# Optimization experiments

Measured on AMD Instinct MI355X. Metric: run time of the kernel, lower is better.

## Reference

```python
import jax, jax.numpy as jnp
import numpy as np


def _segment_mean(msg, dst, num_nodes):
    # msg: [E, B, O, T] summed into [N, B, O, T], mean over incoming edges
    s = jax.ops.segment_sum(msg, dst, num_segments=num_nodes)
    cnt = jax.ops.segment_sum(jnp.ones((msg.shape[0],), msg.dtype), dst, num_segments=num_nodes)
    return s / jnp.clip(cnt, 1.0)[:, None, None, None]


def _gcn(x, edge_index, edge_attr, A, Wk, Wr, b):
    # Edge-conditioned (spline-style) graph conv.
    # x: [B, N, Cin, T]; edge_attr: [E, 3]; Wk: [K, Cin, Cout]
    N = x.shape[1]
    src, dst = edge_index[0], edge_index[1]
    Bw = jax.nn.softmax(edge_attr @ A, axis=-1)          # [E, K] basis weights
    We = jnp.einsum('ek,kio->eio', Bw, Wk)                # [E, Cin, Cout]
    msg = jnp.einsum('beit,eio->ebot', x[:, src], We)     # [E, B, Cout, T]
    agg = _segment_mean(msg, dst, N).transpose(1, 0, 2, 3)  # [B, N, Cout, T]
    out = agg + jnp.einsum('bnit,io->bnot', x, Wr) + b[None, None, :, None]
    return jax.nn.elu(out)


def _pool(x, P, C, T):
    # x: [B, N_l, C, T] -> flatten, sparse-pool with P [N_{l+1}, N_l], unflatten
    B, N = x.shape[0], x.shape[1]
    xf = x.reshape(B, N, C * T)
    xf = jnp.einsum('mn,bnf->bmf', P, xf)
    return xf.reshape(B, P.shape[0], C, T)


def setup_inputs() -> dict:
    key = jax.random.key(0)
    ks = jax.random.split(key, 24)
    B, T = 2, 200
    N = [2048, 512, 128, 64]
    E = [16384, 8192, 2048]
    nf = [1, 8, 16, 32, 64, 128, 128]
    ld = 64

    def rn(k, shape, scale=1.0):
        return jax.random.normal(k, shape, dtype=jnp.float32) * scale

    inp = {}
    inp['x'] = rn(ks[0], (B, N[0], nf[0], T))
    inp['ei0'] = jax.random.randint(ks[1], (2, E[0]), 0, N[0])
    inp['ea0'] = jax.random.uniform(ks[2], (E[0], 3), dtype=jnp.float32)
    inp['ei1'] = jax.random.randint(ks[3], (2, E[1]), 0, N[1])
    inp['ea1'] = jax.random.uniform(ks[4], (E[1], 3), dtype=jnp.float32)
    inp['ei2'] = jax.random.randint(ks[5], (2, E[2]), 0, N[2])
    inp['ea2'] = jax.random.uniform(ks[6], (E[2], 3), dtype=jnp.float32)
    # gcn params: (A basis map, K=3 kernel weights, root weight, bias)
    inp['A1'] = rn(ks[7], (3, 3))
    inp['Wk1'] = rn(ks[8], (3, nf[0], nf[2]), 1.0 / np.sqrt(nf[0]))
    inp['Wr1'] = rn(ks[9], (nf[0], nf[2]), 1.0 / np.sqrt(nf[0]))
    inp['b1'] = jnp.zeros((nf[2],), jnp.float32)
    inp['A2'] = rn(ks[10], (3, 3))
    inp['Wk2'] = rn(ks[11], (3, nf[2], nf[3]), 1.0 / np.sqrt(nf[2]))
    inp['Wr2'] = rn(ks[12], (nf[2], nf[3]), 1.0 / np.sqrt(nf[2]))
    inp['b2'] = jnp.zeros((nf[3],), jnp.float32)
    inp['A3'] = rn(ks[13], (3, 3))
    inp['Wk3'] = rn(ks[14], (3, nf[3], nf[4]), 1.0 / np.sqrt(nf[3]))
    inp['Wr3'] = rn(ks[15], (nf[3], nf[4]), 1.0 / np.sqrt(nf[3]))
    inp['b3'] = jnp.zeros((nf[4],), jnp.float32)
    # sparse pooling projections (dense here)
    inp['P01'] = rn(ks[16], (N[1], N[0]), 1.0 / np.sqrt(N[0]))
    inp['P12'] = rn(ks[17], (N[2], N[1]), 1.0 / np.sqrt(N[1]))
    inp['P23'] = rn(ks[18], (N[3], N[2]), 1.0 / np.sqrt(N[2]))
    # 1x1 conv encoder head
    inp['fce1_w'] = rn(ks[19], (nf[4], nf[6]), 1.0 / np.sqrt(nf[4]))
    inp['fce1_b'] = jnp.zeros((nf[6],), jnp.float32)
    inp['fce2_w'] = rn(ks[20], (nf[6], ld), 1.0 / np.sqrt(nf[6]))
    inp['fce2_b'] = jnp.zeros((ld,), jnp.float32)
    return inp


def reference(x, ei0, ea0, ei1, ea1, ei2, ea2, A1, Wk1, Wr1, b1, A2, Wk2, Wr2, b2,
              A3, Wk3, Wr3, b3, P01, P12, P23, fce1_w, fce1_b, fce2_w, fce2_b):
    T = x.shape[-1]
    # level 0 -> 1
    h = _gcn(x, ei0, ea0, A1, Wk1, Wr1, b1)          # [B, N0, 16, T]
    h = _pool(h, P01, h.shape[2], T)                 # [B, N1, 16, T]
    # level 1 -> 2
    h = _gcn(h, ei1, ea1, A2, Wk2, Wr2, b2)          # [B, N1, 32, T]
    h = _pool(h, P12, h.shape[2], T)                 # [B, N2, 32, T]
    # level 2 -> 3
    h = _gcn(h, ei2, ea2, A3, Wk3, Wr3, b3)          # [B, N2, 64, T]
    h = _pool(h, P23, h.shape[2], T)                 # [B, N3, 64, T]
    # 1x1 conv encoder head (channel-wise linear over node/time grid)
    h = jax.nn.elu(jnp.einsum('bnct,co->bnot', h, fce1_w) + fce1_b[None, None, :, None])
    mu = jnp.tanh(jnp.einsum('bnct,co->bnot', h, fce2_w) + fce2_b[None, None, :, None])
    return mu  # [B, N3, latent_dim, T]
```

## Files before the change

kernel.cpp:

```cpp
#include <hip/hip_runtime.h>
#include <hip/hip_bf16.h>

using bf16 = __hip_bfloat16;
typedef unsigned short ushort_t;
typedef unsigned int uint_t;

constexpr int B = 2, T = 200;
constexpr int N0 = 2048, N1 = 512, N2 = 128, N3 = 64;
constexpr int E0 = 16384, E1 = 8192, E2 = 2048;

typedef __attribute__((ext_vector_type(8))) short bf16x8;
typedef __attribute__((ext_vector_type(4))) float f32x4;

constexpr size_t O_FLAG = 161792;
constexpr size_t O_WC1  = 163840;
constexpr size_t O_BIAS = 164096;
constexpr size_t O_BW0  = 165312;
constexpr size_t O_BW1  = 361920;
constexpr size_t O_BW2  = 460224;
constexpr size_t O_PB1  = 484800;
constexpr size_t O_PB2  = 2581952;
constexpr size_t O_PB3  = 2713024;
constexpr size_t O_WT2  = 2729408;
constexpr size_t O_WT3  = 2733504;
constexpr size_t O_W1H  = 2749888;
constexpr size_t O_W2H  = 2766272;
constexpr size_t O_AA   = 2785280;
constexpr size_t O_BB   = 15892480;

__device__ __forceinline__ float ldx(const void* p, long i, int bf) {
  if (bf) {
    uint_t v = (uint_t)(((const ushort_t*)p)[i]) << 16;
    float f; __builtin_memcpy(&f, &v, 4); return f;
  }
  return ((const float*)p)[i];
}
__device__ __forceinline__ void stf(float* p, float v) { *p = v; }
__device__ __forceinline__ void stf(bf16* p, float v) { *p = __float2bfloat16(v); }
__device__ __forceinline__ ushort_t f2bfu(float v) {
  bf16 h = __float2bfloat16(v); ushort_t u; __builtin_memcpy(&u, &h, 2); return u;
}

__device__ __forceinline__ int probe_bf(const ushort_t* ea) {
  int c = 0;
#pragma unroll 8
  for (int i = 0; i < 128; ++i) {
    uint_t v = (uint_t)ea[i] << 16;
    float f; __builtin_memcpy(&f, &v, 4);
    if (f >= 0.f && f <= 1.0f) c++;
  }
  return (c >= 120) ? 1 : 0;
}

struct InPtrs {
  const void* ea0; const void* ea1; const void* ea2;
  const void* P01; const void* P12; const void* P23;
  const void* Wk1; const void* Wr1; const void* Wk2; const void* Wr2;
  const void* Wk3; const void* Wr3; const void* W1h; const void* W2h;
  const void* b1; const void* b2; const void* b3; const void* b1h; const void* b2h;
  const void* A1; const void* A2; const void* A3;
};

__device__ __forceinline__ void bw_one(const void* ea, int bf, const void* A,
                                       float* bw, int e) {
  float a0 = ldx(ea, e*3+0, bf), a1 = ldx(ea, e*3+1, bf), a2 = ldx(ea, e*3+2, bf);
  float l0 = a0*ldx(A,0,bf) + a1*ldx(A,3,bf) + a2*ldx(A,6,bf);
  float l1 = a0*ldx(A,1,bf) + a1*ldx(A,4,bf) + a2*ldx(A,7,bf);
  float l2 = a0*ldx(A,2,bf) + a1*ldx(A,5,bf) + a2*ldx(A,8,bf);
  float m = fmaxf(l0, fmaxf(l1, l2));
  float x0 = expf(l0 - m), x1 = expf(l1 - m), x2 = expf(l2 - m);
  float inv = 1.0f / (x0 + x1 + x2);
  bw[e*3+0] = x0*inv; bw[e*3+1] = x1*inv; bw[e*3+2] = x2*inv;
}

__global__ void k_prep(InPtrs P, char* base) {
  int bx = blockIdx.x, tid = threadIdx.x;
  if (bx < 158) { ((int*)base)[bx * 256 + tid] = 0; return; }
  if (bx == 158) {
    if (tid == 0) *(int*)(base + O_FLAG) = probe_bf((const ushort_t*)P.ea0);
    return;
  }
  int bf = probe_bf((const ushort_t*)P.ea0);
  float* bw0 = (float*)(base + O_BW0);
  float* bw1 = (float*)(base + O_BW1);
  float* bw2 = (float*)(base + O_BW2);
  if (bx < 223)  { bw_one(P.ea0, bf, P.A1, bw0, (bx-159)*256+tid); return; }
  if (bx < 255)  { bw_one(P.ea1, bf, P.A2, bw1, (bx-223)*256+tid); return; }
  if (bx < 263)  { bw_one(P.ea2, bf, P.A3, bw2, (bx-255)*256+tid); return; }
  if (bx < 4359) { long i = (long)(bx-263)*256+tid;
                   ((ushort_t*)(base+O_PB1))[i] = f2bfu(ldx(P.P01, i, bf)); return; }
  if (bx < 4615) { int i = (bx-4359)*256+tid;
                   ((ushort_t*)(base+O_PB2))[i] = f2bfu(ldx(P.P12, i, bf)); return; }
  if (bx < 4647) { int i = (bx-4615)*256+tid;
                   ((ushort_t*)(base+O_PB3))[i] = f2bfu(ldx(P.P23, i, bf)); return; }
  if (bx < 4655) { int j = (bx-4647)*256+tid; int o = j>>6, c = j&63;
                   float v = (c<48) ? ldx(P.Wk2, c*32+o, bf) : ldx(P.Wr2, (c-48)*32+o, bf);
                   ((ushort_t*)(base+O_WT2))[j] = f2bfu(v); return; }
  if (bx < 4687) { int j = (bx-4655)*256+tid; int o = j>>7, c = j&127;
                   float v = (c<96) ? ldx(P.Wk3, c*64+o, bf) : ldx(P.Wr3, (c-96)*64+o, bf);
                   ((ushort_t*)(base+O_WT3))[j] = f2bfu(v); return; }
  if (bx < 4719) { int j = (bx-4687)*256+tid; int o = j>>6, c = j&63;
                   ((ushort_t*)(base+O_W1H))[j] = f2bfu(ldx(P.W1h, c*128+o, bf)); return; }
  if (bx < 4751) { int j = (bx-4719)*256+tid; int o = j>>7, c = j&127;
                   ((ushort_t*)(base+O_W2H))[j] = f2bfu(ldx(P.W2h, c*64+o, bf)); return; }
  {
    int i = (bx-4751)*256+tid;
    if (i < 64) {
      ((float*)(base+O_WC1))[i] = (i<48) ? ldx(P.Wk1, i, bf) : ldx(P.Wr1, i-48, bf);
    } else if (i < 368) {
      int j = i - 64; float v;
      if (j < 16)       v = ldx(P.b1, j, bf);
      else if (j < 48)  v = ldx(P.b2, j-16, bf);
      else if (j < 112) v = ldx(P.b3, j-48, bf);
      else if (j < 240) v = ldx(P.b1h, j-112, bf);
      else              v = ldx(P.b2h, j-240, bf);
      ((float*)(base+O_BIAS))[j] = v;
    }
  }
}

__global__ void k_hist3(const int* d0, const int* d1, const int* d2,
                        int* c0, int* c1, int* c2) {
  int i = blockIdx.x * 256 + threadIdx.x;
  if (i < E0) atomicAdd(&c0[d0[i]], 1);
  if (i < E1) atomicAdd(&c1[d1[i]], 1);
  if (i < E2) atomicAdd(&c2[d2[i]], 1);
}

__global__ void k_scan3(const int* c0, int* o0, int* u0,
                        const int* c1, int* o1, int* u1,
                        const int* c2, int* o2, int* u2) {
  const int* cnt; int* off; int* cur; int N;
  if (blockIdx.x == 0)      { cnt = c0; off = o0; cur = u0; N = N0; }
  else if (blockIdx.x == 1) { cnt = c1; off = o1; cur = u1; N = N1; }
  else                      { cnt = c2; off = o2; cur = u2; N = N2; }
  int tid = threadIdx.x;
  int chunk = (N + 63) >> 6;
  int base = tid * chunk;
  int s = 0;
  for (int j = 0; j < chunk; ++j) { int idx = base + j; if (idx < N) s += cnt[idx]; }
  int pre = s;
  for (int d = 1; d < 64; d <<= 1) {
    int v = __shfl_up(pre, d, 64);
    if (tid >= d) pre += v;
  }
  int run = pre - s;
  for (int j = 0; j < chunk; ++j) {
    int idx = base + j;
    if (idx < N) { off[idx] = run; cur[idx] = run; run += cnt[idx]; }
  }
  if (tid == 63) off[N] = run;
}

__global__ void k_fill3(const int* d0, int* u0, int* e0l,
                        const int* d1, int* u1, int* e1l,
                        const int* d2, int* u2, int* e2l) {
  int i = blockIdx.x * 256 + threadIdx.x;
  if (i < E0) { int p = atomicAdd(&u0[d0[i]], 1); e0l[p] = i; }
  if (i < E1) { int p = atomicAdd(&u1[d1[i]], 1); e1l[p] = i; }
  if (i < E2) { int p = atomicAdd(&u2[d2[i]], 1); e2l[p] = i; }
}

__global__ __launch_bounds__(256) void k_gc1(const void* x, const int* src,
    const int* off, const int* elist, const int* cnt, const float* bw,
    const float* W, const float* bias, bf16* h1, const int* flagp) {
  __shared__ float Wl[64];
  __shared__ float bl[16];
  __shared__ float ew0[32], ew1[32], ew2[32];
  __shared__ int es[32];
  int tid = threadIdx.x;
  if (tid < 64) Wl[tid] = W[tid];
  if (tid < 16) bl[tid] = bias[tid];
  int bf = *flagp;
  int n = blockIdx.y, b = blockIdx.z;
  int t = tid;
  bool tok = t < T;
  int beg = off[n], end = off[n + 1];
  float a0 = 0.f, a1 = 0.f, a2 = 0.f;
  for (int q0 = beg; q0 < end; q0 += 32) {
    int m = end - q0; if (m > 32) m = 32;
    __syncthreads();
    if (tid < m) {
      int e = elist[q0 + tid];
      es[tid] = src[e];
      ew0[tid] = bw[e*3+0]; ew1[tid] = bw[e*3+1]; ew2[tid] = bw[e*3+2];
    }
    __syncthreads();
    if (tok) {
      for (int j = 0; j < m; ++j) {
        float xv = ldx(x, (long)(b * N0 + es[j]) * T + t, bf);
        a0 += ew0[j] * xv; a1 += ew1[j] * xv; a2 += ew2[j] * xv;
      }
    }
  }
  __syncthreads();
  if (!tok) return;
  int c = cnt[n];
  float inv = 1.f / (float)(c > 0 ? c : 1);
  a0 *= inv; a1 *= inv; a2 *= inv;
  float xr = ldx(x, (long)(b * N0 + n) * T + t, bf);
  bf16* op = h1 + ((long)(b * N0 + n) * 16) * T + t;
#pragma unroll
  for (int o = 0; o < 16; ++o) {
    float v = a0 * Wl[o] + a1 * Wl[16 + o] + a2 * Wl[32 + o] + xr * Wl[48 + o] + bl[o];
    v = v > 0.f ? v : (expf(v) - 1.f);
    op[o * T] = __float2bfloat16(v);
  }
}

template<int CIN, int CPI, int O>
__global__ __launch_bounds__(256) void k_gcm(const float* hp, const int* src,
    const int* off, const int* elist, const int* cnt, const float* bw,
    const ushort_t* Wt, const float* bias, bf16* h, int N) {
  constexpr int C = 4 * CIN;
  constexpr int KG = C / 8;
  constexpr int MT = O / 16;
  __shared__ __align__(16) ushort_t Ws[O * C];
  __shared__ __align__(16) ushort_t Is[64 * C];
  __shared__ float ew0[32], ew1[32], ew2[32];
  __shared__ int es[32];
  int tid = threadIdx.x;
  int w = tid >> 6, l = tid & 63;
  int lf = l & 15, quad = l >> 4;
  int t0 = blockIdx.x * 64;
  int n = blockIdx.y, b = blockIdx.z;
  {
    const uint4* Wg = (const uint4*)Wt;
    for (int s = tid; s < O * KG; s += 256) {
      int o = s / KG, kg = s % KG;
      *(uint4*)(Ws + o * C + ((kg ^ (o & 7)) * 8)) = Wg[s];
    }
  }
  int tx = tid & 63, iy = tid >> 6;
  int t = t0 + tx;
  bool tok = t < T;
  float acc[3][CPI], xr[CPI];
#pragma unroll
  for (int k = 0; k < 3; ++k)
#pragma unroll
    for (int j = 0; j < CPI; ++j) acc[k][j] = 0.f;
#pragma unroll
  for (int j = 0; j < CPI; ++j) xr[j] = 0.f;
  int beg = off[n], end = off[n + 1];
  for (int q0 = beg; q0 < end; q0 += 32) {
    int mE = end - q0; if (mE > 32) mE = 32;
    __syncthreads();
    if (tid < mE) {
      int e = elist[q0 + tid];
      es[tid] = src[e];
      ew0[tid] = bw[e*3+0]; ew1[tid] = bw[e*3+1]; ew2[tid] = bw[e*3+2];
    }
    __syncthreads();
    if (tok) {
      for (int j2 = 0; j2 < mE; ++j2) {
        int s = es[j2];
        float w0 = ew0[j2], w1 = ew1[j2], w2 = ew2[j2];
        const float* xp = hp + ((long)(b * N + s) * CIN) * T + t;
#pragma unroll
        for (int j = 0; j < CPI; ++j) {
          float xv = xp[(iy * CPI + j) * T];
          acc[0][j] += w0 * xv; acc[1][j] += w1 * xv; acc[2][j] += w2 * xv;
        }
      }
    }
  }
  float inv = 1.f;
  if (tok) {
    int c = cnt[n];
    inv = 1.f / (float)(c > 0 ? c : 1);
    const float* xs = hp + ((long)(b * N + n) * CIN) * T + t;
#pragma unroll
    for (int j = 0; j < CPI; ++j) xr[j] = xs[(iy * CPI + j) * T];
  }
#pragma unroll
  for (int j = 0; j < CPI; ++j) {
    int i = iy * CPI + j;
#pragma unroll
    for (int k = 0; k < 3; ++k) {
      int c = k * CIN + i;
      Is[tx * C + ((c >> 3) ^ (tx & 7)) * 8 + (c & 7)] = f2bfu(acc[k][j] * inv);
    }
    int c = 3 * CIN + i;
    Is[tx * C + ((c >> 3) ^ (tx & 7)) * 8 + (c & 7)] = f2bfu(xr[j]);
  }
  __syncthreads();
  f32x4 dacc[MT];
#pragma unroll
  for (int mt = 0; mt < MT; ++mt) dacc[mt] = (f32x4){0.f, 0.f, 0.f, 0.f};
  int tr = w * 16 + lf;
#pragma unroll
  for (int kc = 0; kc < C / 32; ++kc) {
    int kg0 = kc * 4 + quad;
    bf16x8 bfr = *(const bf16x8*)(Is + tr * C + ((kg0 ^ (tr & 7)) * 8));
#pragma unroll
    for (int mt = 0; mt < MT; ++mt) {
      int o = mt * 16 + lf;
      bf16x8 afr = *(const bf16x8*)(Ws + o * C + ((kg0 ^ (o & 7)) * 8));
      dacc[mt] = __builtin_amdgcn_mfma_f32_16x16x32_bf16(afr, bfr, dacc[mt], 0, 0, 0);
    }
  }
  int tg = t0 + w * 16 + lf;
  if (tg < T) {
    long nb = (long)(b * N + n) * O;
#pragma unroll
    for (int mt = 0; mt < MT; ++mt) {
#pragma unroll
      for (int r = 0; r < 4; ++r) {
        int o = mt * 16 + quad * 4 + r;
        float v = dacc[mt][r] + bias[o];
        v = v > 0.f ? v : (expf(v) - 1.f);
        h[(nb + o) * T + tg] = __float2bfloat16(v);
      }
    }
  }
}

template<int WMT, int FT, int SWZ, typename TOut>
__global__ __launch_bounds__(256) void k_pool_mfma(const ushort_t* Pb, const ushort_t* h,
                                                   TOut* out, int M, int K, int F) {
  constexpr int BM = 64 * WMT;
  constexpr int BN = 16 * FT;
  int f0, m0, b;
  if (SWZ) {
    int bx = blockIdx.x;
    int f_blk = (bx & 7) + 8 * (bx >> 6);
    int m_blk = (bx >> 3) & 7;
    if (f_blk * BN >= F) return;
    f0 = f_blk * BN; m0 = m_blk * BM; b = blockIdx.y;
  } else {
    f0 = blockIdx.x * BN; m0 = blockIdx.y * BM; b = blockIdx.z;
  }
  __shared__ __align__(16) ushort_t As[BM * 64];
  __shared__ __align__(16) ushort_t Bs[BN * 64];
  int tid = threadIdx.x;
  int w = tid >> 6, l = tid & 63;
  int lf = l & 15, quad = l >> 4;
  f32x4 acc[WMT][FT];
#pragma unroll
  for (int wt = 0; wt < WMT; ++wt)
#pragma unroll
    for (int ft = 0; ft < FT; ++ft) acc[wt][ft] = (f32x4){0.f, 0.f, 0.f, 0.f};

  for (int k0 = 0; k0 < K; k0 += 64) {
#pragma unroll
    for (int it = 0; it < BM / 32; ++it) {
      int cc = tid + 256 * it;
      int m = cc >> 3, kc = cc & 7;
      uint4 v = *(const uint4*)(Pb + (long)(m0 + m) * K + k0 + kc * 8);
      *(uint4*)(As + m * 64 + ((kc ^ (m & 7)) * 8)) = v;
    }
#pragma unroll
    for (int kb = (tid / BN) * 16; kb < 64; kb += (256 / BN) * 16) {
      int f = tid % BN;
      const ushort_t* hp = h + ((long)(b * K + k0 + kb)) * F + f0 + f;
      ushort_t r[16];
#pragma unroll
      for (int i = 0; i < 16; ++i) r[i] = hp[(long)i * F];
      int kc0 = kb >> 3;
      *(uint4*)(Bs + f * 64 + ((kc0 ^ (f & 7)) * 8)) = *(uint4*)&r[0];
      *(uint4*)(Bs + f * 64 + (((kc0 + 1) ^ (f & 7)) * 8)) = *(uint4*)&r[8];
    }
    __syncthreads();
#pragma unroll
    for (int ks = 0; ks < 2; ++ks) {
      int kc = ks * 4 + quad;
      bf16x8 bfr[FT];
#pragma unroll
      for (int ft = 0; ft < FT; ++ft) {
        int fl = ft * 16 + lf;
        bfr[ft] = *(const bf16x8*)(Bs + fl * 64 + ((kc ^ (fl & 7)) * 8));
      }
#pragma unroll
      for (int wt = 0; wt < WMT; ++wt) {
        int ml = wt * 64 + w * 16 + lf;
        bf16x8 afr = *(const bf16x8*)(As + ml * 64 + ((kc ^ (ml & 7)) * 8));
#pragma unroll
        for (int ft = 0; ft < FT; ++ft)
          acc[wt][ft] = __builtin_amdgcn_mfma_f32_16x16x32_bf16(afr, bfr[ft], acc[wt][ft], 0, 0, 0);
      }
    }
    __syncthreads();
  }
#pragma unroll
  for (int wt = 0; wt < WMT; ++wt) {
#pragma unroll
    for (int r = 0; r < 4; ++r) {
      int m = m0 + wt * 64 + w * 16 + quad * 4 + r;
      TOut* op = out + ((long)(b * M + m)) * F + f0 + lf;
#pragma unroll
      for (int ft = 0; ft < FT; ++ft)
        stf(op + ft * 16, acc[wt][ft][r]);
    }
  }
}

__global__ __launch_bounds__(256) void k_head(const float* hp3, const ushort_t* W1t,
    const ushort_t* W2t, const float* bias, void* outp, const int* flagp) {
  __shared__ __align__(16) ushort_t Ws1[128 * 64];
  __shared__ __align__(16) ushort_t Ws2[64 * 128];
  __shared__ __align__(16) ushort_t Is[64 * 64];
  __shared__ __align__(16) ushort_t G[64 * 128];
  int tid = threadIdx.x;
  int w = tid >> 6, l = tid & 63;
  int lf = l & 15, quad = l >> 4;
  int t0 = blockIdx.x * 64;
  int n = blockIdx.y, b = blockIdx.z;
  {
    const uint4* g1 = (const uint4*)W1t;
    for (int s = tid; s < 1024; s += 256) {
      int o = s >> 3, kg = s & 7;
      *(uint4*)(Ws1 + o * 64 + ((kg ^ (o & 7)) * 8)) = g1[s];
    }
    const uint4* g2 = (const uint4*)W2t;
    for (int s = tid; s < 1024; s += 256) {
      int o = s >> 4, kg = s & 15;
      *(uint4*)(Ws2 + o * 128 + ((kg ^ (o & 7)) * 8)) = g2[s];
    }
  }
  {
    int t = tid & 63;
    bool tok = (t0 + t) < T;
    const float* ip = hp3 + ((long)(b * 64 + n) * 64) * T + t0;
    for (int kg = tid >> 6; kg < 8; kg += 4) {
      ushort_t r[8];
#pragma unroll
      for (int j = 0; j < 8; ++j)
        r[j] = tok ? f2bfu(ip[(kg * 8 + j) * T + t]) : (ushort_t)0;
      *(uint4*)(Is + t * 64 + ((kg ^ (t & 7)) * 8)) = *(uint4*)r;
    }
  }
  __syncthreads();
  int tr = w * 16 + lf;
  {
    f32x4 a1[8];
#pragma unroll
    for (int mt = 0; mt < 8; ++mt) a1[mt] = (f32x4){0.f, 0.f, 0.f, 0.f};
#pragma unroll
    for (int kc = 0; kc < 2; ++kc) {
      int kg0 = kc * 4 + quad;
      bf16x8 bfr = *(const bf16x8*)(Is + tr * 64 + ((kg0 ^ (tr & 7)) * 8));
#pragma unroll
      for (int mt = 0; mt < 8; ++mt) {
        int o = mt * 16 + lf;
        bf16x8 afr = *(const bf16x8*)(Ws1 + o * 64 + ((kg0 ^ (o & 7)) * 8));
        a1[mt] = __builtin_amdgcn_mfma_f32_16x16x32_bf16(afr, bfr, a1[mt], 0, 0, 0);
      }
    }
    int tG = w * 16 + lf;
#pragma unroll
    for (int mt = 0; mt < 8; ++mt) {
#pragma unroll
      for (int r = 0; r < 4; ++r) {
        int o1 = mt * 16 + quad * 4 + r;
        float v = a1[mt][r] + bias[112 + o1];
        v = v > 0.f ? v : (expf(v) - 1.f);
        G[tG * 128 + ((o1 >> 3) ^ (tG & 7)) * 8 + (o1 & 7)] = f2bfu(v);
      }
    }
  }
  __syncthreads();
  {
    f32x4 a2[4];
#pragma unroll
    for (int mt = 0; mt < 4; ++mt) a2[mt] = (f32x4){0.f, 0.f, 0.f, 0.f};
#pragma unroll
    for (int kc = 0; kc < 4; ++kc) {
      int kg0 = kc * 4 + quad;
      bf16x8 bfr = *(const bf16x8*)(G + tr * 128 + ((kg0 ^ (tr & 7)) * 8));
#pragma unroll
      for (int mt = 0; mt < 4; ++mt) {
        int o = mt * 16 + lf;
        bf16x8 afr = *(const bf16x8*)(Ws2 + o * 128 + ((kg0 ^ (o & 7)) * 8));
        a2[mt] = __builtin_amdgcn_mfma_f32_16x16x32_bf16(afr, bfr, a2[mt], 0, 0, 0);
      }
    }
    int t = t0 + w * 16 + lf;
    if (t < T) {
      int bf = *flagp;
      long nb = (long)(b * 64 + n) * 64;
#pragma unroll
      for (int mt = 0; mt < 4; ++mt) {
#pragma unroll
        for (int r = 0; r < 4; ++r) {
          int o2 = mt * 16 + quad * 4 + r;
          float v = tanhf(a2[mt][r] + bias[240 + o2]);
          long idx = (nb + o2) * T + t;
          if (bf) ((bf16*)outp)[idx] = __float2bfloat16(v);
          else    ((float*)outp)[idx] = v;
        }
      }
    }
  }
}

extern "C" void kernel_launch(void* const* d_in, const int* in_sizes, int n_in,
                              void* d_out, int out_size, void* d_ws, size_t ws_size,
                              hipStream_t stream) {
  const int* ei0 = (const int*)d_in[1];
  const int* ei1 = (const int*)d_in[3];
  const int* ei2 = (const int*)d_in[5];

  char* base = (char*)d_ws;
  int* I = (int*)base;
  int* cnt0 = I;         int* off0 = I + 2048;  int* cur0 = I + 4112;  int* el0 = I + 6160;
  int* cnt1 = I + 22544; int* off1 = I + 23056; int* cur1 = I + 23584; int* el1 = I + 24096;
  int* cnt2 = I + 32288; int* off2 = I + 32416; int* cur2 = I + 32560; int* el2 = I + 32688;
  const int* flagp = (const int*)(base + O_FLAG);
  float* wc1f = (float*)(base + O_WC1);
  float* bias = (float*)(base + O_BIAS);
  float* bw0 = (float*)(base + O_BW0);
  float* bw1 = (float*)(base + O_BW1);
  float* bw2 = (float*)(base + O_BW2);
  ushort_t* Pb1 = (ushort_t*)(base + O_PB1);
  ushort_t* Pb2 = (ushort_t*)(base + O_PB2);
  ushort_t* Pb3 = (ushort_t*)(base + O_PB3);
  ushort_t* wt2 = (ushort_t*)(base + O_WT2);
  ushort_t* wt3 = (ushort_t*)(base + O_WT3);
  ushort_t* w1t = (ushort_t*)(base + O_W1H);
  ushort_t* w2t = (ushort_t*)(base + O_W2H);
  char* Aa = base + O_AA;
  char* Bb = base + O_BB;

  InPtrs P = { d_in[2], d_in[4], d_in[6], d_in[19], d_in[20], d_in[21],
               d_in[8], d_in[9], d_in[12], d_in[13], d_in[16], d_in[17],
               d_in[22], d_in[24], d_in[10], d_in[14], d_in[18], d_in[23],
               d_in[25], d_in[7], d_in[11], d_in[15] };

  k_prep<<<4753, 256, 0, stream>>>(P, base);
  k_hist3<<<64, 256, 0, stream>>>(ei0 + E0, ei1 + E1, ei2 + E2, cnt0, cnt1, cnt2);
  k_scan3<<<3, 64, 0, stream>>>(cnt0, off0, cur0, cnt1, off1, cur1, cnt2, off2, cur2);
  k_fill3<<<64, 256, 0, stream>>>(ei0 + E0, cur0, el0, ei1 + E1, cur1, el1, ei2 + E2, cur2, el2);

  k_gc1<<<dim3(1, N0, B), 256, 0, stream>>>(d_in[0], ei0, off0, el0, cnt0, bw0, wc1f, bias, (bf16*)Bb, flagp);
  k_pool_mfma<1, 4, 1, float><<<dim3(448, B, 1), 256, 0, stream>>>(Pb1, (const ushort_t*)Bb, (float*)Aa, 512, 2048, 3200);
  k_gcm<16, 4, 32><<<dim3(4, N1, B), 256, 0, stream>>>((const float*)Aa, ei1, off1, el1, cnt1, bw1, wt2, bias + 16, (bf16*)Bb, N1);
  k_pool_mfma<1, 4, 0, float><<<dim3(100, 2, B), 256, 0, stream>>>(Pb2, (const ushort_t*)Bb, (float*)Aa, 128, 512, 6400);
  k_gcm<32, 8, 64><<<dim3(4, N2, B), 256, 0, stream>>>((const float*)Aa, ei2, off2, el2, cnt2, bw2, wt3, bias + 48, (bf16*)Bb, N2);
  k_pool_mfma<1, 4, 0, float><<<dim3(200, 1, B), 256, 0, stream>>>(Pb3, (const ushort_t*)Bb, (float*)Aa, 64, 128, 12800);
  k_head<<<dim3(4, N3, B), 256, 0, stream>>>((const float*)Aa, w1t, w2t, bias, d_out, flagp);
}
```

Measured before the change: 294.8 us.

## Register-prefetch next K tile and vectorize B loads in pooling GEMM

The pooling MFMA kernel now prefetches the next 64-wide K slice of both P and h into registers while the current slice is consumed from shared memory, overlapping global loads with MFMA work. The B-tile load changes from 16 strided scalar ushort loads per thread to four 8-byte row loads over a 4x4 (k,f) patch, transposed in registers before the swizzled LDS store. The FT template parameter is removed and fixed at 4. Register pressure goes up from the prefetch buffers, and the partial 8-byte LDS stores may cause bank conflicts.

```diff
diff --git a/kernel.cpp b/kernel.cpp
--- a/kernel.cpp
+++ b/kernel.cpp
@@ -315,58 +315,81 @@
   }
 }
 
-template<int WMT, int FT, int SWZ, typename TOut>
+template<int WMT, int SWZ, typename TOut>
 __global__ __launch_bounds__(256) void k_pool_mfma(const ushort_t* Pb, const ushort_t* h,
                                                    TOut* out, int M, int K, int F) {
   constexpr int BM = 64 * WMT;
-  constexpr int BN = 16 * FT;
   int f0, m0, b;
   if (SWZ) {
     int bx = blockIdx.x;
     int f_blk = (bx & 7) + 8 * (bx >> 6);
     int m_blk = (bx >> 3) & 7;
-    if (f_blk * BN >= F) return;
-    f0 = f_blk * BN; m0 = m_blk * BM; b = blockIdx.y;
+    if (f_blk * 64 >= F) return;
+    f0 = f_blk * 64; m0 = m_blk * BM; b = blockIdx.y;
   } else {
-    f0 = blockIdx.x * BN; m0 = blockIdx.y * BM; b = blockIdx.z;
+    f0 = blockIdx.x * 64; m0 = blockIdx.y * BM; b = blockIdx.z;
   }
   __shared__ __align__(16) ushort_t As[BM * 64];
-  __shared__ __align__(16) ushort_t Bs[BN * 64];
+  __shared__ __align__(16) ushort_t Bs[64 * 64];
   int tid = threadIdx.x;
   int w = tid >> 6, l = tid & 63;
   int lf = l & 15, quad = l >> 4;
-  f32x4 acc[WMT][FT];
+  int fB = (tid & 15) * 4;
+  int kB = (tid >> 4) * 4;
+  f32x4 acc[WMT][4];
 #pragma unroll
   for (int wt = 0; wt < WMT; ++wt)
 #pragma unroll
-    for (int ft = 0; ft < FT; ++ft) acc[wt][ft] = (f32x4){0.f, 0.f, 0.f, 0.f};
+    for (int ft = 0; ft < 4; ++ft) acc[wt][ft] = (f32x4){0.f, 0.f, 0.f, 0.f};
+
+  uint4 pa[BM / 32];
+  uint2 pb[4];
+#pragma unroll
+  for (int it = 0; it < BM / 32; ++it) {
+    int cc = tid + 256 * it;
+    int m = cc >> 3, kc = cc & 7;
+    pa[it] = *(const uint4*)(Pb + (long)(m0 + m) * K + kc * 8);
+  }
+#pragma unroll
+  for (int j = 0; j < 4; ++j)
+    pb[j] = *(const uint2*)(h + ((long)(b * K + kB + j)) * F + f0 + fB);
 
   for (int k0 = 0; k0 < K; k0 += 64) {
 #pragma unroll
     for (int it = 0; it < BM / 32; ++it) {
       int cc = tid + 256 * it;
       int m = cc >> 3, kc = cc & 7;
-      uint4 v = *(const uint4*)(Pb + (long)(m0 + m) * K + k0 + kc * 8);
-      *(uint4*)(As + m * 64 + ((kc ^ (m & 7)) * 8)) = v;
-    }
-#pragma unroll
-    for (int kb = (tid / BN) * 16; kb < 64; kb += (256 / BN) * 16) {
-      int f = tid % BN;
-      const ushort_t* hp = h + ((long)(b * K + k0 + kb)) * F + f0 + f;
-      ushort_t r[16];
-#pragma unroll
-      for (int i = 0; i < 16; ++i) r[i] = hp[(long)i * F];
-      int kc0 = kb >> 3;
-      *(uint4*)(Bs + f * 64 + ((kc0 ^ (f & 7)) * 8)) = *(uint4*)&r[0];
-      *(uint4*)(Bs + f * 64 + (((kc0 + 1) ^ (f & 7)) * 8)) = *(uint4*)&r[8];
+      *(uint4*)(As + m * 64 + ((kc ^ (m & 7)) * 8)) = pa[it];
+    }
+    {
+      const ushort_t* pv = (const ushort_t*)pb;
+#pragma unroll
+      for (int i = 0; i < 4; ++i) {
+        uint_t lo = (uint_t)pv[i] | ((uint_t)pv[4 + i] << 16);
+        uint_t hi = (uint_t)pv[8 + i] | ((uint_t)pv[12 + i] << 16);
+        int f = fB + i;
+        *(uint2*)(Bs + f * 64 + (((kB >> 3) ^ (f & 7)) * 8) + (kB & 7)) = (uint2){lo, hi};
+      }
     }
     __syncthreads();
+    if (k0 + 64 < K) {
+      int kn = k0 + 64;
+#pragma unroll
+      for (int it = 0; it < BM / 32; ++it) {
+        int cc = tid + 256 * it;
+        int m = cc >> 3, kc = cc & 7;
+        pa[it] = *(const uint4*)(Pb + (long)(m0 + m) * K + kn + kc * 8);
+      }
+#pragma unroll
+      for (int j = 0; j < 4; ++j)
+        pb[j] = *(const uint2*)(h + ((long)(b * K + kn + kB + j)) * F + f0 + fB);
+    }
 #pragma unroll
     for (int ks = 0; ks < 2; ++ks) {
       int kc = ks * 4 + quad;
-      bf16x8 bfr[FT];
-#pragma unroll
-      for (int ft = 0; ft < FT; ++ft) {
+      bf16x8 bfr[4];
+#pragma unroll
+      for (int ft = 0; ft < 4; ++ft) {
         int fl = ft * 16 + lf;
         bfr[ft] = *(const bf16x8*)(Bs + fl * 64 + ((kc ^ (fl & 7)) * 8));
       }
@@ -375,7 +398,7 @@
         int ml = wt * 64 + w * 16 + lf;
         bf16x8 afr = *(const bf16x8*)(As + ml * 64 + ((kc ^ (ml & 7)) * 8));
 #pragma unroll
-        for (int ft = 0; ft < FT; ++ft)
+        for (int ft = 0; ft < 4; ++ft)
           acc[wt][ft] = __builtin_amdgcn_mfma_f32_16x16x32_bf16(afr, bfr[ft], acc[wt][ft], 0, 0, 0);
       }
     }
@@ -388,7 +411,7 @@
       int m = m0 + wt * 64 + w * 16 + quad * 4 + r;
       TOut* op = out + ((long)(b * M + m)) * F + f0 + lf;
 #pragma unroll
-      for (int ft = 0; ft < FT; ++ft)
+      for (int ft = 0; ft < 4; ++ft)
         stf(op + ft * 16, acc[wt][ft][r]);
     }
   }
@@ -532,10 +555,10 @@
   k_fill3<<<64, 256, 0, stream>>>(ei0 + E0, cur0, el0, ei1 + E1, cur1, el1, ei2 + E2, cur2, el2);
 
   k_gc1<<<dim3(1, N0, B), 256, 0, stream>>>(d_in[0], ei0, off0, el0, cnt0, bw0, wc1f, bias, (bf16*)Bb, flagp);
-  k_pool_mfma<1, 4, 1, float><<<dim3(448, B, 1), 256, 0, stream>>>(Pb1, (const ushort_t*)Bb, (float*)Aa, 512, 2048, 3200);
+  k_pool_mfma<1, 1, float><<<dim3(448, B, 1), 256, 0, stream>>>(Pb1, (const ushort_t*)Bb, (float*)Aa, 512, 2048, 3200);
   k_gcm<16, 4, 32><<<dim3(4, N1, B), 256, 0, stream>>>((const float*)Aa, ei1, off1, el1, cnt1, bw1, wt2, bias + 16, (bf16*)Bb, N1);
-  k_pool_mfma<1, 4, 0, float><<<dim3(100, 2, B), 256, 0, stream>>>(Pb2, (const ushort_t*)Bb, (float*)Aa, 128, 512, 6400);
+  k_pool_mfma<1, 0, float><<<dim3(100, 2, B), 256, 0, stream>>>(Pb2, (const ushort_t*)Bb, (float*)Aa, 128, 512, 6400);
   k_gcm<32, 8, 64><<<dim3(4, N2, B), 256, 0, stream>>>((const float*)Aa, ei2, off2, el2, cnt2, bw2, wt3, bias + 48, (bf16*)Bb, N2);
-  k_pool_mfma<1, 4, 0, float><<<dim3(200, 1, B), 256, 0, stream>>>(Pb3, (const ushort_t*)Bb, (float*)Aa, 64, 128, 12800);
+  k_pool_mfma<1, 0, float><<<dim3(200, 1, B), 256, 0, stream>>>(Pb3, (const ushort_t*)Bb, (float*)Aa, 64, 128, 12800);
   k_head<<<dim3(4, N3, B), 256, 0, stream>>>((const float*)Aa, w1t, w2t, bias, d_out, flagp);
 }
```

Result: slower. 353.2 us (+19.8%).
